# Kernel optimization log

Measured on AMD Instinct MI355X. Metric: run time of the kernel, lower is better.

Reference implementation:

```python
import jax, jax.numpy as jnp
import numpy as np

L = 4096          # total packed length
HID = 2560        # hidden_size
H = 8             # num_attention_heads
KV = 4            # num_key_value_heads
HD = 256          # head_dim
SW = 1024         # sliding_window
SCALING = 256.0 ** -0.5  # query_pre_attn_scalar ** -0.5
EPS = 1e-6
ROPE_BASE = 10000.0


def setup_inputs() -> dict:
    key = jax.random.key(0)
    ks = jax.random.split(key, 9)
    hidden_states = jax.random.normal(ks[0], (L, HID), jnp.float32)
    Wq = jax.random.normal(ks[1], (HID, H * HD), jnp.float32) * 0.02
    Wk = jax.random.normal(ks[2], (HID, KV * HD), jnp.float32) * 0.02
    Wv = jax.random.normal(ks[3], (HID, KV * HD), jnp.float32) * 0.02
    Wo = jax.random.normal(ks[4], (H * HD, HID), jnp.float32) * 0.02
    q_norm_w = jax.random.normal(ks[5], (HD,), jnp.float32) * 0.1
    k_norm_w = jax.random.normal(ks[6], (HD,), jnp.float32) * 0.1
    # 4 packed sequences of length 1024 each; positions restart per sequence
    cu_seqlens = jnp.array([0, 1024, 2048, 3072, 4096], jnp.int32)
    pos = jnp.tile(jnp.arange(1024, dtype=jnp.float32), 4)  # [L]
    inv_freq = 1.0 / (ROPE_BASE ** (jnp.arange(0, HD, 2, dtype=jnp.float32) / HD))
    freqs = pos[:, None] * inv_freq[None, :]                # [L, HD/2]
    emb = jnp.concatenate([freqs, freqs], axis=-1)          # [L, HD]
    cos, sin = jnp.cos(emb), jnp.sin(emb)
    return {"hidden_states": hidden_states, "cos": cos, "sin": sin,
            "Wq": Wq, "Wk": Wk, "Wv": Wv, "Wo": Wo,
            "q_norm_w": q_norm_w, "k_norm_w": k_norm_w,
            "cu_seqlens": cu_seqlens}


def _rotate_half(x):
    x1, x2 = x[..., : HD // 2], x[..., HD // 2:]
    return jnp.concatenate([-x2, x1], axis=-1)


def _rms_norm(x, w):
    # Gemma3RMSNorm: x * rsqrt(mean(x^2) + eps) * (1 + w)
    x32 = x.astype(jnp.float32)
    out = x32 * jax.lax.rsqrt(jnp.mean(x32 * x32, axis=-1, keepdims=True) + EPS)
    return (out * (1.0 + w.astype(jnp.float32))).astype(x.dtype)


def _packed_sliding_causal_mask(cu_seqlens, total_len):
    pos = jnp.arange(total_len)
    seq_ids = jnp.searchsorted(cu_seqlens[1:], pos, side='right')
    seq_mask = seq_ids[:, None] == seq_ids[None, :]
    dist = pos[None, :] - pos[:, None]                      # pos[j] - pos[i]
    causal = dist <= 0
    window = dist >= -(SW - 1)                              # left_window = SW - 1
    keep = seq_mask & causal & window
    return jnp.where(keep, 0.0, -jnp.inf).astype(jnp.float32)  # [L, L]


def reference(hidden_states, cos, sin, Wq, Wk, Wv, Wo, q_norm_w, k_norm_w, cu_seqlens):
    total_len = hidden_states.shape[0]
    # projections -> [n_heads, L, head_dim]
    q = (hidden_states @ Wq).reshape(total_len, H, HD).transpose(1, 0, 2)
    k = (hidden_states @ Wk).reshape(total_len, KV, HD).transpose(1, 0, 2)
    v = (hidden_states @ Wv).reshape(total_len, KV, HD).transpose(1, 0, 2)
    q = _rms_norm(q, q_norm_w)
    k = _rms_norm(k, k_norm_w)
    # RoPE (cos/sin broadcast over heads)
    q = q * cos + _rotate_half(q) * sin
    k = k * cos + _rotate_half(k) * sin
    # GQA repeat_kv: [KV, L, HD] -> [H, L, HD]
    n_rep = H // KV
    k = jnp.repeat(k, n_rep, axis=0)
    v = jnp.repeat(v, n_rep, axis=0)
    mask = _packed_sliding_causal_mask(cu_seqlens, total_len)
    scores = jnp.einsum('hqd,hkd->hqk', q, k) * SCALING + mask[None]
    attn = jax.nn.softmax(scores.astype(jnp.float32), axis=-1).astype(q.dtype)
    out = jnp.einsum('hqk,hkd->qhd', attn, v).reshape(total_len, H * HD)
    return out @ Wo  # [L, hidden]
```

## Files before the change

### kernel.cpp

```cpp
#include <hip/hip_runtime.h>
#include <hip/hip_bf16.h>

typedef unsigned short u16;
typedef float f32x4 __attribute__((ext_vector_type(4)));
typedef short bf16x8 __attribute__((ext_vector_type(8)));

__device__ __forceinline__ float bf2f(u16 u) {
    union { float f; unsigned int i; } c; c.i = ((unsigned int)u) << 16; return c.f;
}
__device__ __forceinline__ u16 f2bf(float f) {
    union { float f; unsigned int i; } c; c.f = f;
    unsigned int r = c.i + 0x7fffu + ((c.i >> 16) & 1u);
    return (u16)(r >> 16);
}
__device__ __forceinline__ void gload16(const void* g, void* l) {
    __builtin_amdgcn_global_load_lds(
        (const __attribute__((address_space(1))) void*)g,
        (__attribute__((address_space(3))) void*)l, 16, 0, 0);
}

__device__ __forceinline__ void dev_tr_f32_bf16(
    const float* __restrict__ in, u16* __restrict__ out, int R, int C,
    int bx, int by)
{
    __shared__ u16 tile[32][34];
    const int tx = threadIdx.x & 31;
    const int ty = threadIdx.x >> 5;
    const size_t r0 = (size_t)by * 32;
    const size_t c0 = (size_t)bx * 32;
#pragma unroll
    for (int i = 0; i < 4; ++i) {
        int r = ty + 8 * i;
        tile[r][tx] = f2bf(in[(r0 + r) * C + c0 + tx]);
    }
    __syncthreads();
#pragma unroll
    for (int i = 0; i < 4; ++i) {
        int r = ty + 8 * i;
        out[(c0 + r) * R + r0 + tx] = tile[tx][r];
    }
}

__global__ __launch_bounds__(256) void prep_all(
    const float* __restrict__ hid, u16* __restrict__ hidb,
    const float* __restrict__ Wq, const float* __restrict__ Wk,
    const float* __restrict__ Wv, const float* __restrict__ Wo,
    u16* __restrict__ WqkvT, u16* __restrict__ WoT)
{
    const int b = blockIdx.x;
    if (b < 5120) {
        int i = b * 256 + threadIdx.x;
        const float4 a = *(const float4*)&hid[(size_t)i * 8];
        const float4 v = *(const float4*)&hid[(size_t)i * 8 + 4];
        bf16x8 o;
        o[0] = (short)f2bf(a.x); o[1] = (short)f2bf(a.y);
        o[2] = (short)f2bf(a.z); o[3] = (short)f2bf(a.w);
        o[4] = (short)f2bf(v.x); o[5] = (short)f2bf(v.y);
        o[6] = (short)f2bf(v.z); o[7] = (short)f2bf(v.w);
        *(bf16x8*)&hidb[(size_t)i * 8] = o;
    } else if (b < 10240) {
        int id = b - 5120;
        dev_tr_f32_bf16(Wq, WqkvT, 2560, 2048, id % 64, id / 64);
    } else if (b < 12800) {
        int id = b - 10240;
        dev_tr_f32_bf16(Wk, WqkvT + (size_t)2048 * 2560, 2560, 1024, id % 32, id / 32);
    } else if (b < 15360) {
        int id = b - 12800;
        dev_tr_f32_bf16(Wv, WqkvT + (size_t)3072 * 2560, 2560, 1024, id % 32, id / 32);
    } else {
        int id = b - 15360;
        dev_tr_f32_bf16(Wo, WoT, 2048, 2560, id % 80, id / 80);
    }
}

template<typename TOUT>
__global__ __launch_bounds__(512, 2) void gemm_bt8p(
    const u16* __restrict__ A, const u16* __restrict__ Bt, TOUT* __restrict__ C,
    int M, int N, int K)
{
    __shared__ u16 As[2][2][128 * 64];
    __shared__ u16 Bs[2][2][128 * 64];
    const int tid  = threadIdx.x;
    const int lane = tid & 63;
    const int w    = tid >> 6;
    const int wm   = w >> 2;
    const int wn   = w & 3;
    const int g    = lane >> 4, c = lane & 15;

    const int nbx = gridDim.x;
    int lin = blockIdx.y * nbx + blockIdx.x;
    const int cpx = (nbx * gridDim.y) >> 3;
    lin = (lin & 7) * cpx + (lin >> 3);
    const size_t mbase = (size_t)(lin / nbx) * 256;
    const size_t nbase = (size_t)(lin % nbx) * 256;

    const int srow0 = lane >> 3;
    const int sslot = lane & 7;
    const int swz   = (sslot ^ srow0) << 3;

    auto stageG = [&](int t, int qg) {
        const int half = w >> 2;
        const int ch   = qg * 4 + (w & 3);
        const int rw   = ch * 8 + srow0;
        gload16(A + (mbase + half * 128 + rw) * (size_t)K + t * 64 + swz,
                &As[t & 1][half][ch * 512]);
    };
    auto stageB4 = [&](int t) {
#pragma unroll
        for (int i = 0; i < 4; ++i) {
            const int gc   = w * 4 + i;
            const int half = gc >> 4;
            const int ch   = gc & 15;
            const int rw   = ch * 8 + srow0;
            gload16(Bt + (nbase + half * 128 + rw) * (size_t)K + t * 64 + swz,
                    &Bs[t & 1][half][ch * 512]);
        }
    };
    auto ldA = [&](int t, int m, int kk) -> bf16x8 {
        const int r = m * 16 + c;
        return *(const bf16x8*)&As[t & 1][wm][r * 64 + ((kk * 32 + g * 8) ^ ((r & 7) << 3))];
    };
    auto ldB = [&](int t, int n, int kk) -> bf16x8 {
        const int r = (wn & 1) * 64 + n * 16 + c;
        return *(const bf16x8*)&Bs[t & 1][wn >> 1][r * 64 + ((kk * 32 + g * 8) ^ ((r & 7) << 3))];
    };

    f32x4 acc[8][4];
#pragma unroll
    for (int m = 0; m < 8; ++m)
#pragma unroll
        for (int n = 0; n < 4; ++n) { acc[m][n][0]=0.f; acc[m][n][1]=0.f; acc[m][n][2]=0.f; acc[m][n][3]=0.f; }

    const int nT = K >> 6;

    stageG(0, 3); stageB4(0); stageG(0, 0); stageG(0, 1); stageG(0, 2);
    asm volatile("s_waitcnt vmcnt(2)" ::: "memory");
    __builtin_amdgcn_sched_barrier(0);
    __builtin_amdgcn_s_barrier();

    for (int t = 0; t < nT; ++t) {
        bf16x8 bF[4][2], aF[2][2];
        const bool more = (t + 1 < nT);

#pragma unroll
        for (int n = 0; n < 4; ++n) { bF[n][0] = ldB(t, n, 0); bF[n][1] = ldB(t, n, 1); }
#pragma unroll
        for (int i = 0; i < 2; ++i) { aF[i][0] = ldA(t, i, 0); aF[i][1] = ldA(t, i, 1); }
        if (more) stageG(t + 1, 3);
        __builtin_amdgcn_s_barrier();
        __builtin_amdgcn_s_setprio(1);
#pragma unroll
        for (int kk = 0; kk < 2; ++kk)
#pragma unroll
            for (int i = 0; i < 2; ++i)
#pragma unroll
                for (int n = 0; n < 4; ++n)
                    acc[i][n] = __builtin_amdgcn_mfma_f32_16x16x32_bf16(
                        aF[i][kk], bF[n][kk], acc[i][n], 0, 0, 0);
        __builtin_amdgcn_s_setprio(0);
        if (more) asm volatile("s_waitcnt vmcnt(2)" ::: "memory");
        else      asm volatile("s_waitcnt vmcnt(1)" ::: "memory");
        __builtin_amdgcn_sched_barrier(0);
        __builtin_amdgcn_s_barrier();

#pragma unroll
        for (int i = 0; i < 2; ++i) { aF[i][0] = ldA(t, 2 + i, 0); aF[i][1] = ldA(t, 2 + i, 1); }
        if (more) stageB4(t + 1);
        __builtin_amdgcn_s_barrier();
        __builtin_amdgcn_s_setprio(1);
#pragma unroll
        for (int kk = 0; kk < 2; ++kk)
#pragma unroll
            for (int i = 0; i < 2; ++i)
#pragma unroll
                for (int n = 0; n < 4; ++n)
                    acc[2 + i][n] = __builtin_amdgcn_mfma_f32_16x16x32_bf16(
                        aF[i][kk], bF[n][kk], acc[2 + i][n], 0, 0, 0);
        __builtin_amdgcn_s_setprio(0);
        if (more) asm volatile("s_waitcnt vmcnt(5)" ::: "memory");
        else      asm volatile("s_waitcnt vmcnt(0)" ::: "memory");
        __builtin_amdgcn_sched_barrier(0);
        __builtin_amdgcn_s_barrier();

#pragma unroll
        for (int i = 0; i < 2; ++i) { aF[i][0] = ldA(t, 4 + i, 0); aF[i][1] = ldA(t, 4 + i, 1); }
        if (more) stageG(t + 1, 0);
        __builtin_amdgcn_s_barrier();
        __builtin_amdgcn_s_setprio(1);
#pragma unroll
        for (int kk = 0; kk < 2; ++kk)
#pragma unroll
            for (int i = 0; i < 2; ++i)
#pragma unroll
                for (int n = 0; n < 4; ++n)
                    acc[4 + i][n] = __builtin_amdgcn_mfma_f32_16x16x32_bf16(
                        aF[i][kk], bF[n][kk], acc[4 + i][n], 0, 0, 0);
        __builtin_amdgcn_s_setprio(0);
        __builtin_amdgcn_s_barrier();

#pragma unroll
        for (int i = 0; i < 2; ++i) { aF[i][0] = ldA(t, 6 + i, 0); aF[i][1] = ldA(t, 6 + i, 1); }
        if (more) { stageG(t + 1, 1); stageG(t + 1, 2); }
        __builtin_amdgcn_s_barrier();
        __builtin_amdgcn_s_setprio(1);
#pragma unroll
        for (int kk = 0; kk < 2; ++kk)
#pragma unroll
            for (int i = 0; i < 2; ++i)
#pragma unroll
                for (int n = 0; n < 4; ++n)
                    acc[6 + i][n] = __builtin_amdgcn_mfma_f32_16x16x32_bf16(
                        aF[i][kk], bF[n][kk], acc[6 + i][n], 0, 0, 0);
        __builtin_amdgcn_s_setprio(0);
        if (more) {
            asm volatile("s_waitcnt vmcnt(2)" ::: "memory");
            __builtin_amdgcn_sched_barrier(0);
        }
        __builtin_amdgcn_s_barrier();
    }

#pragma unroll
    for (int m = 0; m < 8; ++m)
#pragma unroll
        for (int n = 0; n < 4; ++n)
#pragma unroll
            for (int i = 0; i < 4; ++i) {
                size_t r   = mbase + wm * 128 + m * 16 + g * 4 + i;
                size_t col = nbase + wn * 64 + n * 16 + c;
                if constexpr (sizeof(TOUT) == 4) C[r * (size_t)N + col] = acc[m][n][i];
                else                             C[r * (size_t)N + col] = f2bf(acc[m][n][i]);
            }
}

__device__ __forceinline__ void dev_rmsnorm_rope(
    u16* __restrict__ buf, int ld, const float* __restrict__ wgt,
    const float* __restrict__ cosb, const float* __restrict__ sinb,
    int heads, float outscale, int blk)
{
    const int lane = threadIdx.x & 63;
    const int wv   = threadIdx.x >> 6;
    const int rid  = blk * 4 + wv;
    const int t    = rid / heads;
    const int h    = rid - t * heads;
    u16* p = buf + (size_t)t * ld + h * 256 + lane * 4;

    ushort4 xu = *(const ushort4*)p;
    float x0 = bf2f(xu.x), x1 = bf2f(xu.y), x2 = bf2f(xu.z), x3 = bf2f(xu.w);
    float ss = x0*x0 + x1*x1 + x2*x2 + x3*x3;
#pragma unroll
    for (int msk = 1; msk < 64; msk <<= 1) ss += __shfl_xor(ss, msk);
    const float rstd = rsqrtf(ss * (1.0f / 256.0f) + 1e-6f);

    const int d0 = lane * 4;
    const float4 wv4 = *(const float4*)&wgt[d0];
    float xn0 = x0 * rstd * (1.0f + wv4.x);
    float xn1 = x1 * rstd * (1.0f + wv4.y);
    float xn2 = x2 * rstd * (1.0f + wv4.z);
    float xn3 = x3 * rstd * (1.0f + wv4.w);

    float pn0 = __shfl_xor(xn0, 32);
    float pn1 = __shfl_xor(xn1, 32);
    float pn2 = __shfl_xor(xn2, 32);
    float pn3 = __shfl_xor(xn3, 32);
    const float sgn = (lane < 32) ? -1.0f : 1.0f;

    const float4 cv = *(const float4*)&cosb[(size_t)t * 256 + d0];
    const float4 sv = *(const float4*)&sinb[(size_t)t * 256 + d0];
    float r0 = (xn0 * cv.x + sgn * pn0 * sv.x) * outscale;
    float r1 = (xn1 * cv.y + sgn * pn1 * sv.y) * outscale;
    float r2 = (xn2 * cv.z + sgn * pn2 * sv.z) * outscale;
    float r3 = (xn3 * cv.w + sgn * pn3 * sv.w) * outscale;

    ushort4 ou;
    ou.x = f2bf(r0); ou.y = f2bf(r1); ou.z = f2bf(r2); ou.w = f2bf(r3);
    *(ushort4*)p = ou;
}

__global__ __launch_bounds__(256) void postqkv(
    u16* __restrict__ qkv, const float* __restrict__ qnw,
    const float* __restrict__ knw, const float* __restrict__ cosb,
    const float* __restrict__ sinb, u16* __restrict__ vT)
{
    const int b = blockIdx.x;
    if (b < 8192) {
        dev_rmsnorm_rope(qkv, 4096, qnw, cosb, sinb, 8, 0.0625f, b);
    } else if (b < 12288) {
        dev_rmsnorm_rope(qkv + 2048, 4096, knw, cosb, sinb, 4, 1.0f, b - 8192);
    } else {
        __shared__ u16 tile[32][34];
        const int id = b - 12288;
        const int bx = id & 31, by = id >> 5;
        const int tx = threadIdx.x & 31;
        const int ty = threadIdx.x >> 5;
        const size_t r0 = (size_t)by * 32;
        const size_t c0 = (size_t)bx * 32;
        const u16* in = qkv + 3072;
#pragma unroll
        for (int i = 0; i < 4; ++i) {
            int r = ty + 8 * i;
            tile[r][tx] = in[(r0 + r) * 4096 + c0 + tx];
        }
        __syncthreads();
#pragma unroll
        for (int i = 0; i < 4; ++i) {
            int r = ty + 8 * i;
            vT[(c0 + r) * 4096 + r0 + tx] = tile[tx][r];
        }
    }
}

__global__ __launch_bounds__(512, 2) void attn_kernel(
    const u16* __restrict__ q, int ldq,
    const u16* __restrict__ k, int ldk,
    const u16* __restrict__ vT,
    u16* __restrict__ Opart,
    float* __restrict__ stats)
{
    __shared__ u16 Ks[2][32 * 256];
    __shared__ u16 Vs[256 * 40];
    __shared__ u16 P[8][16][56];
    __shared__ float corrsF[8][16];
    const int tid  = threadIdx.x;
    const int lane = tid & 63;
    const int w    = tid >> 6;
    const int g    = lane >> 4, c = lane & 15;
    const int s    = blockIdx.y;
    const int kvh  = blockIdx.z & 3;
    const int kvs  = blockIdx.z >> 2;
    const int qt   = kvs ? (int)blockIdx.x : 15 - (int)blockIdx.x;
    const int h    = kvh * 2 + (w >> 2);
    const int seq0 = s << 10;
    const int qrow0 = qt * 64 + (w & 3) * 16;
    const float NEG = -3.0e38f;

    bf16x8 qf[8];
    {
        const u16* qp = q + (size_t)(seq0 + qrow0 + c) * ldq + h * 256 + g * 8;
#pragma unroll
        for (int ch = 0; ch < 8; ++ch) qf[ch] = *(const bf16x8*)(qp + ch * 32);
    }

    const int kchunk0  = w * 2;
    const int krow_in  = (lane >> 5);
    const int kcol_lin = (lane & 31) * 16;
    const u16* kbase = k + (size_t)seq0 * ldk + kvh * 256;
    const int vd  = tid & 255;
    const int vj0 = (tid >> 8) * 2;
    const int vsw = (vd >> 3) & 3;
    const u16* vbase = vT + ((size_t)kvh * 256 + vd) * 4096 + seq0 + vj0 * 8;

    f32x4 oacc[16];
#pragma unroll
    for (int dt = 0; dt < 16; ++dt) { oacc[dt][0]=0.f; oacc[dt][1]=0.f; oacc[dt][2]=0.f; oacc[dt][3]=0.f; }
    float mq = -1e30f;
    float lq = 0.f;

    const int nt = qt + 1;
    const int t0 = kvs * nt;

    bf16x8 vreg[2];
#pragma unroll
    for (int i = 0; i < 2; ++i) {
        const int chunk = kchunk0 + i;
        const int row   = chunk * 2 + krow_in;
        const int bcol  = kcol_lin ^ ((row & 7) << 4);
        gload16(kbase + (size_t)(t0 * 32 + row) * ldk + (bcol >> 1), &Ks[0][chunk * 512]);
    }
#pragma unroll
    for (int j = 0; j < 2; ++j) vreg[j] = *(const bf16x8*)(vbase + t0 * 32 + j * 8);
    __syncthreads();
#pragma unroll
    for (int j = 0; j < 2; ++j)
        *(bf16x8*)&Vs[vd * 40 + (((vj0 + j) ^ vsw) * 8)] = vreg[j];
    __syncthreads();

    for (int ti = 0; ti < nt; ++ti) {
        const int p   = ti & 1;
        const int kv0 = (t0 + ti) * 32;

        if (ti + 1 < nt) {
#pragma unroll
            for (int i = 0; i < 2; ++i) {
                const int chunk = kchunk0 + i;
                const int row   = chunk * 2 + krow_in;
                const int bcol  = kcol_lin ^ ((row & 7) << 4);
                gload16(kbase + (size_t)(kv0 + 32 + row) * ldk + (bcol >> 1),
                        &Ks[p ^ 1][chunk * 512]);
            }
#pragma unroll
            for (int j = 0; j < 2; ++j) vreg[j] = *(const bf16x8*)(vbase + kv0 + 32 + j * 8);
        }

        f32x4 sacc[2];
#pragma unroll
        for (int nh = 0; nh < 2; ++nh) { sacc[nh][0]=0.f; sacc[nh][1]=0.f; sacc[nh][2]=0.f; sacc[nh][3]=0.f; }
        __builtin_amdgcn_s_setprio(1);
#pragma unroll
        for (int nh = 0; nh < 2; ++nh) {
            const int krow = nh * 16 + c;
#pragma unroll
            for (int ch = 0; ch < 8; ++ch) {
                const int sw = ((ch * 64 + g * 16) ^ ((c & 7) << 4)) >> 1;
                bf16x8 kf = *(const bf16x8*)&Ks[p][krow * 256 + sw];
                sacc[nh] = __builtin_amdgcn_mfma_f32_16x16x32_bf16(kf, qf[ch], sacc[nh], 0, 0, 0);
            }
        }
        __builtin_amdgcn_s_setprio(0);

        const int qloc = qrow0 + c;
        float pmax = NEG;
#pragma unroll
        for (int nh = 0; nh < 2; ++nh)
#pragma unroll
            for (int i = 0; i < 4; ++i) {
                if (kv0 + nh * 16 + g * 4 + i > qloc) sacc[nh][i] = NEG;
                pmax = fmaxf(pmax, sacc[nh][i]);
            }
        pmax = fmaxf(pmax, __shfl_xor(pmax, 16));
        pmax = fmaxf(pmax, __shfl_xor(pmax, 32));

        const bool rescale = !__all(pmax - mq <= 8.0f);
        float corr = 1.0f;
        if (rescale) {
            const float mn = fmaxf(mq, pmax);
            corr = __expf(mq - mn);
            mq = mn;
            if (g == 0) corrsF[w][c] = corr;
        }

        float rowsum = 0.f;
        unsigned int pw[4];
#pragma unroll
        for (int nh = 0; nh < 2; ++nh) {
            float p0 = __expf(sacc[nh][0] - mq);
            float p1 = __expf(sacc[nh][1] - mq);
            float p2 = __expf(sacc[nh][2] - mq);
            float p3 = __expf(sacc[nh][3] - mq);
            rowsum += (p0 + p1) + (p2 + p3);
            pw[nh * 2 + 0] = (unsigned int)f2bf(p0) | ((unsigned int)f2bf(p1) << 16);
            pw[nh * 2 + 1] = (unsigned int)f2bf(p2) | ((unsigned int)f2bf(p3) << 16);
        }
#pragma unroll
        for (int nh = 0; nh < 2; ++nh) {
            *(unsigned int*)&P[w][c][nh * 16 + g * 4]     = pw[nh * 2 + 0];
            *(unsigned int*)&P[w][c][nh * 16 + g * 4 + 2] = pw[nh * 2 + 1];
        }
        rowsum += __shfl_xor(rowsum, 16);
        rowsum += __shfl_xor(rowsum, 32);
        lq = lq * corr + rowsum;

        bf16x8 pf = *(const bf16x8*)&P[w][c][g * 8];

        if (rescale) {
            const f32x4 c4 = *(const f32x4*)&corrsF[w][g * 4];
#pragma unroll
            for (int dt = 0; dt < 16; ++dt)
#pragma unroll
                for (int i = 0; i < 4; ++i) oacc[dt][i] *= c4[i];
        }

        __builtin_amdgcn_s_setprio(1);
#pragma unroll
        for (int dt = 0; dt < 16; ++dt) {
            const int d = dt * 16 + c;
            bf16x8 vf = *(const bf16x8*)&Vs[d * 40 + ((g ^ ((d >> 3) & 3)) * 8)];
            oacc[dt] = __builtin_amdgcn_mfma_f32_16x16x32_bf16(pf, vf, oacc[dt], 0, 0, 0);
        }
        __builtin_amdgcn_s_setprio(0);

        __syncthreads();
        if (ti + 1 < nt) {
#pragma unroll
            for (int j = 0; j < 2; ++j)
                *(bf16x8*)&Vs[vd * 40 + (((vj0 + j) ^ vsw) * 8)] = vreg[j];
        }
        __syncthreads();
    }

    u16* op = Opart + (size_t)kvs * 4096 * 2048;
#pragma unroll
    for (int dt = 0; dt < 16; ++dt)
#pragma unroll
        for (int i = 0; i < 4; ++i)
            op[(size_t)(seq0 + qrow0 + g * 4 + i) * 2048 + h * 256 + dt * 16 + c] =
                f2bf(oacc[dt][i]);
    if (g == 0) {
        const int row = seq0 + qrow0 + c;
        stats[(((size_t)kvs * 8 + h) * 2 + 0) * 4096 + row] = mq;
        stats[(((size_t)kvs * 8 + h) * 2 + 1) * 4096 + row] = lq;
    }
}

__global__ __launch_bounds__(256) void merge_partial(
    const u16* __restrict__ Op,
    const float* __restrict__ stats,
    u16* __restrict__ ob)
{
    const int idx = blockIdx.x * 256 + threadIdx.x;
    const int row = idx >> 8;
    const int col = (idx & 255) * 8;
    const int h   = col >> 8;
    const float m0 = stats[((0 * 8 + h) * 2 + 0) * 4096 + row];
    const float l0 = stats[((0 * 8 + h) * 2 + 1) * 4096 + row];
    const float m1 = stats[((1 * 8 + h) * 2 + 0) * 4096 + row];
    const float l1 = stats[((1 * 8 + h) * 2 + 1) * 4096 + row];
    const float mm = fmaxf(m0, m1);
    const float w0 = __expf(m0 - mm);
    const float w1 = __expf(m1 - mm);
    const float inv = 1.0f / (w0 * l0 + w1 * l1);
    const float s0 = w0 * inv, s1 = w1 * inv;
    const size_t base = (size_t)row * 2048 + col;
    bf16x8 a = *(const bf16x8*)&Op[base];
    bf16x8 b = *(const bf16x8*)&Op[(size_t)4096 * 2048 + base];
    bf16x8 r;
#pragma unroll
    for (int j = 0; j < 8; ++j)
        r[j] = (short)f2bf(bf2f((u16)a[j]) * s0 + bf2f((u16)b[j]) * s1);
    *(bf16x8*)&ob[base] = r;
}

extern "C" void kernel_launch(void* const* d_in, const int* in_sizes, int n_in,
                              void* d_out, int out_size, void* d_ws, size_t ws_size,
                              hipStream_t stream)
{
    const float* hid  = (const float*)d_in[0];
    const float* cosb = (const float*)d_in[1];
    const float* sinb = (const float*)d_in[2];
    const float* Wq   = (const float*)d_in[3];
    const float* Wk   = (const float*)d_in[4];
    const float* Wv   = (const float*)d_in[5];
    const float* Wo   = (const float*)d_in[6];
    const float* qnw  = (const float*)d_in[7];
    const float* knw  = (const float*)d_in[8];

    char* ws = (char*)d_ws;
    const size_t R1 = 0;
    const size_t R2 = (size_t)4096 * 2560 * 2;
    const size_t R3 = R2 * 2;
    u16* hidb  = (u16*)(ws + R1);
    u16* WoT   = (u16*)(ws + R1);
    u16* vT    = (u16*)(ws + R1 + (size_t)2560 * 2048 * 2);
    u16* WqkvT = (u16*)(ws + R2);
    u16* ob    = (u16*)(ws + R2);
    u16* qkv   = (u16*)(ws + R3);
    float* stats = (float*)(ws + R3 + (size_t)4096 * 4096 * 2);
    u16* WoT2  = (u16*)(ws + R3 + (size_t)4096 * 4096 * 2 + (1 << 20));
    u16* Opart = (u16*)d_out;
    (void)ws_size; (void)in_sizes; (void)n_in; (void)out_size;
    WoT = WoT2;

    dim3 B(256);
    prep_all<<<dim3(20480), B, 0, stream>>>(hid, hidb, Wq, Wk, Wv, Wo, WqkvT, WoT);

    gemm_bt8p<u16><<<dim3(16, 16), dim3(512), 0, stream>>>(hidb, WqkvT, qkv, 4096, 4096, 2560);

    postqkv<<<dim3(16384), B, 0, stream>>>(qkv, qnw, knw, cosb, sinb, vT);

    attn_kernel<<<dim3(16, 4, 8), dim3(512), 0, stream>>>(qkv, 4096, qkv + 2048, 4096, vT,
                                                          Opart, stats);
    merge_partial<<<dim3(4096), B, 0, stream>>>(Opart, stats, ob);

    gemm_bt8p<float><<<dim3(10, 16), dim3(512), 0, stream>>>(ob, WoT, (float*)d_out, 4096, 2560, 2048);
}
```

Baseline: 263.9 us.

## Reorder GEMM k-loop phases and load V directly from global in attention

The GEMM main loop is reorganised into four phases that each handle one k-half across four m-tiles, with B staging split into two halves. This reduces fragment register pressure and spreads the global-to-LDS loads more evenly. In the attention kernel, the V tile no longer goes through shared memory: each lane reads V fragments straight from global into registers. That removes the V LDS stores and one __syncthreads per iteration, but adds global load latency and register use. A leftover workspace pointer alias is also cleaned up.

Result: slower. 295.0 us (+11.8%).

```diff
diff --git a/kernel.cpp b/kernel.cpp
--- a/kernel.cpp
+++ b/kernel.cpp
@@ -105,10 +105,10 @@
         gload16(A + (mbase + half * 128 + rw) * (size_t)K + t * 64 + swz,
                 &As[t & 1][half][ch * 512]);
     };
-    auto stageB4 = [&](int t) {
-#pragma unroll
-        for (int i = 0; i < 4; ++i) {
-            const int gc   = w * 4 + i;
+    auto stageB2 = [&](int t, int h2) {
+#pragma unroll
+        for (int i = 0; i < 2; ++i) {
+            const int gc   = w * 4 + h2 * 2 + i;
             const int half = gc >> 4;
             const int ch   = gc & 15;
             const int rw   = ch * 8 + srow0;
@@ -133,84 +133,76 @@
 
     const int nT = K >> 6;
 
-    stageG(0, 3); stageB4(0); stageG(0, 0); stageG(0, 1); stageG(0, 2);
+    stageB2(0, 0); stageB2(0, 1);
+    stageG(0, 0); stageG(0, 1); stageG(0, 2); stageG(0, 3);
     asm volatile("s_waitcnt vmcnt(2)" ::: "memory");
     __builtin_amdgcn_sched_barrier(0);
     __builtin_amdgcn_s_barrier();
 
     for (int t = 0; t < nT; ++t) {
-        bf16x8 bF[4][2], aF[2][2];
+        bf16x8 b0[4], b1[4], a4[4];
         const bool more = (t + 1 < nT);
 
 #pragma unroll
-        for (int n = 0; n < 4; ++n) { bF[n][0] = ldB(t, n, 0); bF[n][1] = ldB(t, n, 1); }
-#pragma unroll
-        for (int i = 0; i < 2; ++i) { aF[i][0] = ldA(t, i, 0); aF[i][1] = ldA(t, i, 1); }
-        if (more) stageG(t + 1, 3);
+        for (int n = 0; n < 4; ++n) b0[n] = ldB(t, n, 0);
+#pragma unroll
+        for (int m = 0; m < 4; ++m) a4[m] = ldA(t, m, 0);
+        if (more) stageB2(t + 1, 0);
         __builtin_amdgcn_s_barrier();
         __builtin_amdgcn_s_setprio(1);
 #pragma unroll
-        for (int kk = 0; kk < 2; ++kk)
-#pragma unroll
-            for (int i = 0; i < 2; ++i)
-#pragma unroll
-                for (int n = 0; n < 4; ++n)
-                    acc[i][n] = __builtin_amdgcn_mfma_f32_16x16x32_bf16(
-                        aF[i][kk], bF[n][kk], acc[i][n], 0, 0, 0);
+        for (int m = 0; m < 4; ++m)
+#pragma unroll
+            for (int n = 0; n < 4; ++n)
+                acc[m][n] = __builtin_amdgcn_mfma_f32_16x16x32_bf16(
+                    a4[m], b0[n], acc[m][n], 0, 0, 0);
         __builtin_amdgcn_s_setprio(0);
-        if (more) asm volatile("s_waitcnt vmcnt(2)" ::: "memory");
-        else      asm volatile("s_waitcnt vmcnt(1)" ::: "memory");
-        __builtin_amdgcn_sched_barrier(0);
-        __builtin_amdgcn_s_barrier();
-
-#pragma unroll
-        for (int i = 0; i < 2; ++i) { aF[i][0] = ldA(t, 2 + i, 0); aF[i][1] = ldA(t, 2 + i, 1); }
-        if (more) stageB4(t + 1);
+        __builtin_amdgcn_s_barrier();
+
+#pragma unroll
+        for (int n = 0; n < 4; ++n) b1[n] = ldB(t, n, 1);
+#pragma unroll
+        for (int m = 0; m < 4; ++m) a4[m] = ldA(t, m, 1);
+        if (more) stageB2(t + 1, 1);
         __builtin_amdgcn_s_barrier();
         __builtin_amdgcn_s_setprio(1);
 #pragma unroll
-        for (int kk = 0; kk < 2; ++kk)
-#pragma unroll
-            for (int i = 0; i < 2; ++i)
-#pragma unroll
-                for (int n = 0; n < 4; ++n)
-                    acc[2 + i][n] = __builtin_amdgcn_mfma_f32_16x16x32_bf16(
-                        aF[i][kk], bF[n][kk], acc[2 + i][n], 0, 0, 0);
+        for (int m = 0; m < 4; ++m)
+#pragma unroll
+            for (int n = 0; n < 4; ++n)
+                acc[m][n] = __builtin_amdgcn_mfma_f32_16x16x32_bf16(
+                    a4[m], b1[n], acc[m][n], 0, 0, 0);
         __builtin_amdgcn_s_setprio(0);
-        if (more) asm volatile("s_waitcnt vmcnt(5)" ::: "memory");
+        __builtin_amdgcn_s_barrier();
+
+        if (more) asm volatile("s_waitcnt vmcnt(4)" ::: "memory");
         else      asm volatile("s_waitcnt vmcnt(0)" ::: "memory");
         __builtin_amdgcn_sched_barrier(0);
-        __builtin_amdgcn_s_barrier();
-
-#pragma unroll
-        for (int i = 0; i < 2; ++i) { aF[i][0] = ldA(t, 4 + i, 0); aF[i][1] = ldA(t, 4 + i, 1); }
-        if (more) stageG(t + 1, 0);
+#pragma unroll
+        for (int m = 0; m < 4; ++m) a4[m] = ldA(t, 4 + m, 0);
+        if (more) { stageG(t + 1, 0); stageG(t + 1, 1); }
         __builtin_amdgcn_s_barrier();
         __builtin_amdgcn_s_setprio(1);
 #pragma unroll
-        for (int kk = 0; kk < 2; ++kk)
-#pragma unroll
-            for (int i = 0; i < 2; ++i)
-#pragma unroll
-                for (int n = 0; n < 4; ++n)
-                    acc[4 + i][n] = __builtin_amdgcn_mfma_f32_16x16x32_bf16(
-                        aF[i][kk], bF[n][kk], acc[4 + i][n], 0, 0, 0);
+        for (int m = 0; m < 4; ++m)
+#pragma unroll
+            for (int n = 0; n < 4; ++n)
+                acc[4 + m][n] = __builtin_amdgcn_mfma_f32_16x16x32_bf16(
+                    a4[m], b0[n], acc[4 + m][n], 0, 0, 0);
         __builtin_amdgcn_s_setprio(0);
         __builtin_amdgcn_s_barrier();
 
 #pragma unroll
-        for (int i = 0; i < 2; ++i) { aF[i][0] = ldA(t, 6 + i, 0); aF[i][1] = ldA(t, 6 + i, 1); }
-        if (more) { stageG(t + 1, 1); stageG(t + 1, 2); }
+        for (int m = 0; m < 4; ++m) a4[m] = ldA(t, 4 + m, 1);
+        if (more) { stageG(t + 1, 2); stageG(t + 1, 3); }
         __builtin_amdgcn_s_barrier();
         __builtin_amdgcn_s_setprio(1);
 #pragma unroll
-        for (int kk = 0; kk < 2; ++kk)
-#pragma unroll
-            for (int i = 0; i < 2; ++i)
-#pragma unroll
-                for (int n = 0; n < 4; ++n)
-                    acc[6 + i][n] = __builtin_amdgcn_mfma_f32_16x16x32_bf16(
-                        aF[i][kk], bF[n][kk], acc[6 + i][n], 0, 0, 0);
+        for (int m = 0; m < 4; ++m)
+#pragma unroll
+            for (int n = 0; n < 4; ++n)
+                acc[4 + m][n] = __builtin_amdgcn_mfma_f32_16x16x32_bf16(
+                    a4[m], b1[n], acc[4 + m][n], 0, 0, 0);
         __builtin_amdgcn_s_setprio(0);
         if (more) {
             asm volatile("s_waitcnt vmcnt(2)" ::: "memory");
@@ -317,7 +309,6 @@
     float* __restrict__ stats)
 {
     __shared__ u16 Ks[2][32 * 256];
-    __shared__ u16 Vs[256 * 40];
     __shared__ u16 P[8][16][56];
     __shared__ float corrsF[8][16];
     const int tid  = threadIdx.x;
@@ -344,10 +335,7 @@
     const int krow_in  = (lane >> 5);
     const int kcol_lin = (lane & 31) * 16;
     const u16* kbase = k + (size_t)seq0 * ldk + kvh * 256;
-    const int vd  = tid & 255;
-    const int vj0 = (tid >> 8) * 2;
-    const int vsw = (vd >> 3) & 3;
-    const u16* vbase = vT + ((size_t)kvh * 256 + vd) * 4096 + seq0 + vj0 * 8;
+    const u16* vrow = vT + ((size_t)kvh * 256 + c) * 4096 + seq0;
 
     f32x4 oacc[16];
 #pragma unroll
@@ -358,7 +346,6 @@
     const int nt = qt + 1;
     const int t0 = kvs * nt;
 
-    bf16x8 vreg[2];
 #pragma unroll
     for (int i = 0; i < 2; ++i) {
         const int chunk = kchunk0 + i;
@@ -366,12 +353,6 @@
         const int bcol  = kcol_lin ^ ((row & 7) << 4);
         gload16(kbase + (size_t)(t0 * 32 + row) * ldk + (bcol >> 1), &Ks[0][chunk * 512]);
     }
-#pragma unroll
-    for (int j = 0; j < 2; ++j) vreg[j] = *(const bf16x8*)(vbase + t0 * 32 + j * 8);
-    __syncthreads();
-#pragma unroll
-    for (int j = 0; j < 2; ++j)
-        *(bf16x8*)&Vs[vd * 40 + (((vj0 + j) ^ vsw) * 8)] = vreg[j];
     __syncthreads();
 
     for (int ti = 0; ti < nt; ++ti) {
@@ -387,9 +368,12 @@
                 gload16(kbase + (size_t)(kv0 + 32 + row) * ldk + (bcol >> 1),
                         &Ks[p ^ 1][chunk * 512]);
             }
-#pragma unroll
-            for (int j = 0; j < 2; ++j) vreg[j] = *(const bf16x8*)(vbase + kv0 + 32 + j * 8);
-        }
+        }
+
+        bf16x8 v0[8], v1[8];
+#pragma unroll
+        for (int dt = 0; dt < 8; ++dt)
+            v0[dt] = *(const bf16x8*)(vrow + (size_t)dt * 16 * 4096 + kv0 + g * 8);
 
         f32x4 sacc[2];
 #pragma unroll
@@ -406,6 +390,10 @@
             }
         }
         __builtin_amdgcn_s_setprio(0);
+
+#pragma unroll
+        for (int dt = 0; dt < 8; ++dt)
+            v1[dt] = *(const bf16x8*)(vrow + (size_t)(dt + 8) * 16 * 4096 + kv0 + g * 8);
 
         const int qloc = qrow0 + c;
         float pmax = NEG;
@@ -461,19 +449,13 @@
 
         __builtin_amdgcn_s_setprio(1);
 #pragma unroll
-        for (int dt = 0; dt < 16; ++dt) {
-            const int d = dt * 16 + c;
-            bf16x8 vf = *(const bf16x8*)&Vs[d * 40 + ((g ^ ((d >> 3) & 3)) * 8)];
-            oacc[dt] = __builtin_amdgcn_mfma_f32_16x16x32_bf16(pf, vf, oacc[dt], 0, 0, 0);
-        }
+        for (int dt = 0; dt < 8; ++dt)
+            oacc[dt] = __builtin_amdgcn_mfma_f32_16x16x32_bf16(pf, v0[dt], oacc[dt], 0, 0, 0);
+#pragma unroll
+        for (int dt = 0; dt < 8; ++dt)
+            oacc[8 + dt] = __builtin_amdgcn_mfma_f32_16x16x32_bf16(pf, v1[dt], oacc[8 + dt], 0, 0, 0);
         __builtin_amdgcn_s_setprio(0);
 
-        __syncthreads();
-        if (ti + 1 < nt) {
-#pragma unroll
-            for (int j = 0; j < 2; ++j)
-                *(bf16x8*)&Vs[vd * 40 + (((vj0 + j) ^ vsw) * 8)] = vreg[j];
-        }
         __syncthreads();
     }
 
@@ -538,16 +520,14 @@
     const size_t R2 = (size_t)4096 * 2560 * 2;
     const size_t R3 = R2 * 2;
     u16* hidb  = (u16*)(ws + R1);
-    u16* WoT   = (u16*)(ws + R1);
     u16* vT    = (u16*)(ws + R1 + (size_t)2560 * 2048 * 2);
     u16* WqkvT = (u16*)(ws + R2);
     u16* ob    = (u16*)(ws + R2);
     u16* qkv   = (u16*)(ws + R3);
     float* stats = (float*)(ws + R3 + (size_t)4096 * 4096 * 2);
-    u16* WoT2  = (u16*)(ws + R3 + (size_t)4096 * 4096 * 2 + (1 << 20));
+    u16* WoT   = (u16*)(ws + R3 + (size_t)4096 * 4096 * 2 + (1 << 20));
     u16* Opart = (u16*)d_out;
     (void)ws_size; (void)in_sizes; (void)n_in; (void)out_size;
-    WoT = WoT2;
 
     dim3 B(256);
     prep_all<<<dim3(20480), B, 0, stream>>>(hid, hidb, Wq, Wk, Wv, Wo, WqkvT, WoT);
```
